# Kernel tuning notes

Measured on AMD Instinct MI355X. Metric: run time of the kernel, lower is better.

Reference implementation:

```python
import jax, jax.numpy as jnp
import numpy as np

D_MODEL = 1024
HEAD_DIM = 128
SEQ_LEN = 4096
BATCH = 4


def setup_inputs() -> dict:
    key = jax.random.key(0)
    kx, kq, kk, kv, ko = jax.random.split(key, 5)
    s = 1.0 / np.sqrt(D_MODEL)
    so = 1.0 / np.sqrt(HEAD_DIM)
    return {
        "x": jax.random.normal(kx, (SEQ_LEN, BATCH, D_MODEL), dtype=jnp.float32),
        "Wq": jax.random.uniform(kq, (HEAD_DIM, D_MODEL), jnp.float32, -s, s),
        "Wk": jax.random.uniform(kk, (HEAD_DIM, D_MODEL), jnp.float32, -s, s),
        "Wv": jax.random.uniform(kv, (HEAD_DIM, D_MODEL), jnp.float32, -s, s),
        "Wo": jax.random.uniform(ko, (D_MODEL, HEAD_DIM), jnp.float32, -so, so),
    }


def reference(x, Wq, Wk, Wv, Wo):
    # x: (S, B, D)
    S = x.shape[0]
    scale = Wq.shape[0] ** (-0.5)  # head_dim ** -0.5
    # Projections (Linear: x @ W.T) -> (B, S, H)
    Q = jnp.einsum('sbd,hd->bsh', x, Wq)
    K = jnp.einsum('sbd,hd->bsh', x, Wk)
    V = jnp.einsum('sbd,hd->bsh', x, Wv)
    scores = jnp.einsum('bqh,bkh->bqk', Q, K) * scale  # (B, S, S)
    causal = jnp.tril(jnp.ones((S, S), dtype=bool))
    scores = jnp.where(causal[None], scores, -jnp.inf)
    attn = jax.nn.softmax(scores, axis=-1)
    attn = jnp.nan_to_num(attn, nan=0.0)
    out = jnp.einsum('bqk,bkh->bqh', attn, V)  # (B, S, H)
    # out_proj then back to (S, B, D)
    return jnp.einsum('bsh,dh->sbd', out, Wo)
```

## Files before the change

### kernel.cpp

```cpp
#include <hip/hip_runtime.h>
#include <hip/hip_bf16.h>

#define S_LEN 4096
#define BATCH 4
#define DMODEL 1024
#define HDIM 128
#define NSLOT 4

typedef __attribute__((ext_vector_type(8))) short short8;
typedef __attribute__((ext_vector_type(4))) short short4v;
typedef __attribute__((ext_vector_type(4))) float float4v;
typedef __attribute__((ext_vector_type(16))) float float16v;
typedef __attribute__((ext_vector_type(4))) int int4v;

#define MASKVAL (-3.0e38f)
#define MINIT   (-1.0e30f)

static __device__ __forceinline__ unsigned short f2bf(float f) {
    __hip_bfloat16 h = __float2bfloat16(f);
    return *reinterpret_cast<unsigned short*>(&h);
}
static __device__ __forceinline__ unsigned short f2h(float f) {
    _Float16 h = (_Float16)f; return *reinterpret_cast<unsigned short*>(&h);
}
static __device__ __forceinline__ float h2f(unsigned short u) {
    _Float16 h = *reinterpret_cast<_Float16*>(&u); return (float)h;
}

__global__ __launch_bounds__(256) void xprep_kernel(
    const float* __restrict__ x, unsigned short* __restrict__ xf)
{
    int n = blockIdx.x * 256 + threadIdx.x;
    int b = n >> 17;
    int rem = n & 131071;
    int sb = rem >> 10;
    int rem2 = rem & 1023;
    int kq = rem2 >> 4;
    int grp = rem2 & 15;
    int lane0 = grp * 4;
    int par = grp >> 3;
    int s0 = lane0 & 31;
    int k = kq * 16 + par * 8;

    short8 hv[4];
#pragma unroll
    for (int r = 0; r < 4; r++) {
        int s = sb * 32 + s0 + r;
        const float* src = &x[((size_t)s * BATCH + b) * DMODEL + k];
        float4 v0 = *reinterpret_cast<const float4*>(src);
        float4 v1 = *reinterpret_cast<const float4*>(src + 4);
        short8 h;
        h[0] = (short)f2bf(v0.x); h[1] = (short)f2bf(v0.y);
        h[2] = (short)f2bf(v0.z); h[3] = (short)f2bf(v0.w);
        h[4] = (short)f2bf(v1.x); h[5] = (short)f2bf(v1.y);
        h[6] = (short)f2bf(v1.z); h[7] = (short)f2bf(v1.w);
        hv[r] = h;
    }
    size_t addr = (((size_t)b * 128 + sb) * 64 + kq) * 512 + (size_t)lane0 * 8;
#pragma unroll
    for (int r = 0; r < 4; r++)
        *reinterpret_cast<short8*>(xf + addr + r * 8) = hv[r];
}

__global__ __launch_bounds__(256) void wprep_kernel(
    const float* __restrict__ Wq, const float* __restrict__ Wk,
    const float* __restrict__ Wv, unsigned short* __restrict__ Wqf,
    unsigned short* __restrict__ Wkf, unsigned short* __restrict__ Wvf)
{
    const int which = blockIdx.y;
    const float* W = (which == 0) ? Wq : (which == 1) ? Wk : Wv;
    unsigned short* Wf = (which == 0) ? Wqf : (which == 1) ? Wkf : Wvf;
    int n = blockIdx.x * 256 + threadIdx.x;
    int d = n >> 7, k8 = n & 127;
    const float* src = &W[(size_t)d * DMODEL + k8 * 8];
    float4 v0 = *reinterpret_cast<const float4*>(src);
    float4 v1 = *reinterpret_cast<const float4*>(src + 4);
    short8 h;
    h[0] = (short)f2bf(v0.x); h[1] = (short)f2bf(v0.y);
    h[2] = (short)f2bf(v0.z); h[3] = (short)f2bf(v0.w);
    h[4] = (short)f2bf(v1.x); h[5] = (short)f2bf(v1.y);
    h[6] = (short)f2bf(v1.z); h[7] = (short)f2bf(v1.w);
    size_t addr = (((size_t)(d >> 5)) * 64 + (k8 >> 1)) * 512
                + (size_t)(((d & 31) + 32 * (k8 & 1)) * 8);
    *reinterpret_cast<short8*>(Wf + addr) = h;
}

__global__ __launch_bounds__(256, 4) void qkv_gemm_kernel(
    const unsigned short* __restrict__ xf, const unsigned short* __restrict__ Wqf,
    const unsigned short* __restrict__ Wkf, const unsigned short* __restrict__ Wvf,
    unsigned short* __restrict__ Qf, unsigned short* __restrict__ Kf,
    unsigned short* __restrict__ Vf)
{
    __shared__ float cacc[2 * 4096];

    const int t = threadIdx.x;
    const int w = t >> 6;
    const int lane = t & 63;
    const int hi = lane >> 5;
    const int tloc = w & 1;
    const int half = w >> 1;
    const int tile = blockIdx.x * 2 + tloc;
    const int which = tile >> 9;
    const int rem = tile & 511;
    const int b = rem >> 7;
    const int sblk = rem & 127;

    const unsigned short* Wf = (which == 0) ? Wqf : (which == 1) ? Wkf : Wvf;
    const unsigned short* xp =
        xf + (((size_t)b * 128 + sblk) * 64 + half * 32) * 512 + lane * 8;
    const unsigned short* wp = Wf + (size_t)half * 32 * 512 + lane * 8;

    float16v acc[4];
#pragma unroll
    for (int i = 0; i < 4; i++)
#pragma unroll
        for (int r = 0; r < 16; r++) acc[i][r] = 0.f;

    if (which != 2) {
#pragma unroll 2
        for (int ks = 0; ks < 32; ks++) {
            short8 xv = *reinterpret_cast<const short8*>(xp + ks * 512);
#pragma unroll
            for (int db = 0; db < 4; db++) {
                short8 wv = *reinterpret_cast<const short8*>(
                    wp + (size_t)(db * 64 + ks) * 512);
                acc[db] = __builtin_amdgcn_mfma_f32_32x32x16_bf16(
                    wv, xv, acc[db], 0, 0, 0);
            }
        }
    } else {
#pragma unroll 2
        for (int ks = 0; ks < 32; ks++) {
            short8 xv = *reinterpret_cast<const short8*>(xp + ks * 512);
#pragma unroll
            for (int hb = 0; hb < 4; hb++) {
                short8 wv = *reinterpret_cast<const short8*>(
                    wp + (size_t)(hb * 64 + ks) * 512);
                acc[hb] = __builtin_amdgcn_mfma_f32_32x32x16_bf16(
                    xv, wv, acc[hb], 0, 0, 0);
            }
        }
    }

    float* my = cacc + tloc * 4096;
    if (half == 1) {
#pragma unroll
        for (int db = 0; db < 4; db++)
#pragma unroll
            for (int rc = 0; rc < 4; rc++) {
                float4v v;
#pragma unroll
                for (int j = 0; j < 4; j++) v[j] = acc[db][rc * 4 + j];
                *reinterpret_cast<float4v*>(
                    my + (db * 4 + rc) * 256 + lane * 4) = v;
            }
    }
    __syncthreads();
    if (half != 0) return;

#pragma unroll
    for (int db = 0; db < 4; db++)
#pragma unroll
        for (int rc = 0; rc < 4; rc++) {
            float4v v = *reinterpret_cast<const float4v*>(
                my + (db * 4 + rc) * 256 + lane * 4);
#pragma unroll
            for (int j = 0; j < 4; j++) acc[db][rc * 4 + j] += v[j];
        }

    if (which != 2) {
        unsigned short* Of = (which == 0) ? Qf : Kf;
        const float scale = (which == 0) ? 0.08838834764831845f : 1.0f;
#pragma unroll
        for (int db = 0; db < 4; db++)
#pragma unroll
            for (int g = 0; g < 4; g++) {
                int f = db * 2 + (g >> 1);
                size_t addr = (((size_t)b * 128 + sblk) * 8 + f) * 512
                            + (size_t)(((lane & 31) + 32 * (g & 1)) * 8 + 4 * hi);
                short4v ov;
#pragma unroll
                for (int j = 0; j < 4; j++)
                    ov[j] = (short)f2bf(acc[db][g * 4 + j] * scale);
                *reinterpret_cast<short4v*>(Of + addr) = ov;
            }
    } else {
#pragma unroll
        for (int hb = 0; hb < 4; hb++)
#pragma unroll
            for (int g = 0; g < 4; g++) {
                int kt16 = sblk * 2 + (g >> 1);
                size_t addr = (((size_t)b * 256 + kt16) * 4 + hb) * 512
                            + (size_t)(((lane & 31) + 32 * (g & 1)) * 8 + 4 * hi);
                short4v ov;
#pragma unroll
                for (int j = 0; j < 4; j++)
                    ov[j] = (short)f2bf(acc[hb][g * 4 + j]);
                *reinterpret_cast<short4v*>(Vf + addr) = ov;
            }
    }
}

__global__ __launch_bounds__(256) void attn_kernel(
    const unsigned short* __restrict__ Qf, const unsigned short* __restrict__ Kf,
    const unsigned short* __restrict__ Vf, unsigned short* __restrict__ Opart,
    float* __restrict__ Mpart, float* __restrict__ Lpart)
{
    const int t = threadIdx.x;
    const int w = t >> 6;
    const int lane = t & 63;
    const int l31 = lane & 31;
    const int hi = lane >> 5;

    const int i = blockIdx.x;
    const int xx = i & 7, j = i >> 3;
    const int b = xx >> 1;
    const int p = j * 2 + (xx & 1);
    const int qt = 31 - (p & 31);
    const int c = p >> 5;

    const int nkv = 2 * (qt + 1);
    const int csize = (nkv + NSLOT - 1) / NSLOT;
    const int lo = c * csize;
    const int hic = min(lo + csize, nkv);
    if (lo >= hic) return;

    const int qb = qt * 128;
    const int qrow = qb + w * 32 + l31;

    const unsigned short* qp =
        Qf + (((size_t)b * 128 + (qt * 4 + w)) * 8) * 512 + lane * 8;
    short8 qf[8];
#pragma unroll
    for (int f = 0; f < 8; f++)
        qf[f] = *reinterpret_cast<const short8*>(qp + f * 512);

    const unsigned short* kbase =
        Kf + (size_t)b * (S_LEN / 32) * 8 * 512 + lane * 8;
    const unsigned short* vbase =
        Vf + (size_t)b * (S_LEN / 16) * 4 * 512 + lane * 8;

    float m_run = MINIT, l_run = 0.f;
    float16v o[4];
#pragma unroll
    for (int hb = 0; hb < 4; hb++)
#pragma unroll
        for (int r = 0; r < 16; r++) o[hb][r] = 0.f;

    for (int ti = lo; ti < hic; ti++) {
        const int kvb = ti * 64;
        const unsigned short* kp = kbase + (size_t)ti * 8192;

        float16v s0, s1;
#pragma unroll
        for (int r = 0; r < 16; r++) { s0[r] = 0.f; s1[r] = 0.f; }
#pragma unroll
        for (int f = 0; f < 8; f++) {
            short8 k0 = *reinterpret_cast<const short8*>(kp + f * 512);
            short8 k1 = *reinterpret_cast<const short8*>(kp + 4096 + f * 512);
            s0 = __builtin_amdgcn_mfma_f32_32x32x16_bf16(k0, qf[f], s0, 0, 0, 0);
            s1 = __builtin_amdgcn_mfma_f32_32x32x16_bf16(k1, qf[f], s1, 0, 0, 0);
        }

        if (kvb + 63 > qb + w * 32) {
#pragma unroll
            for (int r = 0; r < 16; r++) {
                int kv0 = kvb + (r & 3) + 8 * (r >> 2) + 4 * hi;
                if (kv0 > qrow) s0[r] = MASKVAL;
                if (kv0 + 32 > qrow) s1[r] = MASKVAL;
            }
        }

        float pmax = s0[0];
#pragma unroll
        for (int r = 1; r < 16; r++) pmax = fmaxf(pmax, s0[r]);
#pragma unroll
        for (int r = 0; r < 16; r++) pmax = fmaxf(pmax, s1[r]);
        pmax = fmaxf(pmax, __shfl_xor(pmax, 32));
        float mnew = fmaxf(m_run, pmax);
        float alpha = __expf(m_run - mnew);
        m_run = mnew;
#pragma unroll
        for (int r = 0; r < 16; r++) s0[r] = __expf(s0[r] - mnew);
#pragma unroll
        for (int r = 0; r < 16; r++) s1[r] = __expf(s1[r] - mnew);
        float sum = 0.f;
#pragma unroll
        for (int r = 0; r < 16; r++) sum += s0[r] + s1[r];
        sum += __shfl_xor(sum, 32);
        l_run = l_run * alpha + sum;
#pragma unroll
        for (int hb = 0; hb < 4; hb++) o[hb] = o[hb] * alpha;

        const unsigned short* vp = vbase + (size_t)ti * 8192;
#pragma unroll
        for (int tw = 0; tw < 4; tw++) {
            float pv[8];
#pragma unroll
            for (int jj = 0; jj < 8; jj++)
                pv[jj] = (tw < 2) ? ((tw & 1) ? s0[8 + jj] : s0[jj])
                                  : ((tw & 1) ? s1[8 + jj] : s1[jj]);
            unsigned int A  = (unsigned int)f2bf(pv[0]) | ((unsigned int)f2bf(pv[1]) << 16);
            unsigned int Bw = (unsigned int)f2bf(pv[2]) | ((unsigned int)f2bf(pv[3]) << 16);
            unsigned int C  = (unsigned int)f2bf(pv[4]) | ((unsigned int)f2bf(pv[5]) << 16);
            unsigned int D  = (unsigned int)f2bf(pv[6]) | ((unsigned int)f2bf(pv[7]) << 16);
            unsigned int y1 = (unsigned int)__shfl_xor((int)(hi ? A : C), 32);
            unsigned int y2 = (unsigned int)__shfl_xor((int)(hi ? Bw : D), 32);
            int4v pw;
            pw[0] = (int)(hi ? y1 : A);
            pw[1] = (int)(hi ? y2 : Bw);
            pw[2] = (int)(hi ? C : y1);
            pw[3] = (int)(hi ? D : y2);
            union { int4v iv; short8 s; } pu; pu.iv = pw;
#pragma unroll
            for (int hb = 0; hb < 4; hb++) {
                short8 vf = *reinterpret_cast<const short8*>(
                    vp + (tw * 4 + hb) * 512);
                o[hb] = __builtin_amdgcn_mfma_f32_32x32x16_bf16(vf, pu.s, o[hb], 0, 0, 0);
            }
        }
    }

    const size_t R0 = (size_t)(c * BATCH + b) * S_LEN;
    const float inv = (l_run > 0.f) ? 1.f / l_run : 0.f;
#pragma unroll
    for (int hb = 0; hb < 4; hb++)
#pragma unroll
        for (int g = 0; g < 4; g++) {
            int h0 = hb * 32 + g * 8 + hi * 4;
            short4v ov;
#pragma unroll
            for (int jj = 0; jj < 4; jj++)
                ov[jj] = (short)f2h(o[hb][g * 4 + jj] * inv);
            *reinterpret_cast<short4v*>(&Opart[(R0 + qrow) * HDIM + h0]) = ov;
        }
    if (hi == 0) { Mpart[R0 + qrow] = m_run; Lpart[R0 + qrow] = l_run; }
}

__global__ __launch_bounds__(256) void combine_kernel(
    const unsigned short* __restrict__ Opart, const float* __restrict__ Mpart,
    const float* __restrict__ Lpart, unsigned short* __restrict__ Ob)
{
    const int BS = BATCH * S_LEN;
    int idx = blockIdx.x * 256 + threadIdx.x;
    int r = idx >> 4, hc = (idx & 15) * 8;
    int q = r & (S_LEN - 1);
    int qt = q >> 7;
    int nkv = 2 * (qt + 1);
    int csize = (nkv + NSLOT - 1) / NSLOT;
    int cnt = (nkv + csize - 1) / csize;

    float m = -INFINITY;
    for (int j = 0; j < cnt; j++) m = fmaxf(m, Mpart[j * BS + r]);
    float wsum = 0.f;
    float acc[8];
#pragma unroll
    for (int e = 0; e < 8; e++) acc[e] = 0.f;
    for (int j = 0; j < cnt; j++) {
        float wj = __expf(Mpart[j * BS + r] - m) * Lpart[j * BS + r];
        wsum += wj;
        short8 o = *reinterpret_cast<const short8*>(
            &Opart[((size_t)j * BS + r) * HDIM + hc]);
#pragma unroll
        for (int e = 0; e < 8; e++) acc[e] += wj * h2f((unsigned short)o[e]);
    }
    float inv = 1.f / wsum;
    short8 ob;
#pragma unroll
    for (int e = 0; e < 8; e++) ob[e] = (short)f2bf(acc[e] * inv);
    *reinterpret_cast<short8*>(&Ob[(size_t)r * HDIM + hc]) = ob;
}

__global__ __launch_bounds__(256) void out_proj_kernel(
    const unsigned short* __restrict__ Ob, const float* __restrict__ Wo,
    float* __restrict__ out)
{
    __shared__ unsigned short As[128 * 128];
    __shared__ unsigned short Bs[128 * 128];

    const int t = threadIdx.x;
    const int lane = t & 63, w = t >> 6;
    const int l15 = lane & 15, l4 = lane >> 4;
    const int wr = (w >> 1) * 64, wc = (w & 1) * 64;
    const int s0 = blockIdx.x * 128;
    const int d0 = blockIdx.y * 128;
    const int b = blockIdx.z;

#pragma unroll
    for (int p = 0; p < 8; p++) {
        int e = p * 2048 + t * 8;
        int r = e >> 7, h = e & 127;
        short8 v = *reinterpret_cast<const short8*>(
            &Ob[((size_t)b * S_LEN + s0 + r) * HDIM + h]);
        int off = (r * 256 + h * 2) ^ ((r & 7) << 4);
        *reinterpret_cast<short8*>(reinterpret_cast<char*>(As) + off) = v;
    }
#pragma unroll
    for (int p = 0; p < 16; p++) {
        int e = p * 1024 + t * 4;
        int r = e >> 7, h = e & 127;
        float4 v = *reinterpret_cast<const float4*>(&Wo[(size_t)(d0 + r) * HDIM + h]);
        short4v hh;
        hh[0] = (short)f2bf(v.x); hh[1] = (short)f2bf(v.y);
        hh[2] = (short)f2bf(v.z); hh[3] = (short)f2bf(v.w);
        int off = (r * 256 + h * 2) ^ ((r & 7) << 4);
        *reinterpret_cast<short4v*>(reinterpret_cast<char*>(Bs) + off) = hh;
    }
    __syncthreads();

    float4v acc[4][4];
#pragma unroll
    for (int i = 0; i < 4; i++)
#pragma unroll
        for (int j = 0; j < 4; j++) acc[i][j] = (float4v){0.f, 0.f, 0.f, 0.f};

#pragma unroll
    for (int kk = 0; kk < 4; kk++) {
        short8 a[4], bf[4];
#pragma unroll
        for (int mi = 0; mi < 4; mi++) {
            int row = wr + mi * 16 + l15;
            int off = (row * 256 + (kk * 32 + l4 * 8) * 2) ^ ((row & 7) << 4);
            a[mi] = *reinterpret_cast<const short8*>(
                reinterpret_cast<const char*>(As) + off);
        }
#pragma unroll
        for (int ni = 0; ni < 4; ni++) {
            int row = wc + ni * 16 + l15;
            int off = (row * 256 + (kk * 32 + l4 * 8) * 2) ^ ((row & 7) << 4);
            bf[ni] = *reinterpret_cast<const short8*>(
                reinterpret_cast<const char*>(Bs) + off);
        }
#pragma unroll
        for (int mi = 0; mi < 4; mi++)
#pragma unroll
            for (int ni = 0; ni < 4; ni++)
                acc[mi][ni] = __builtin_amdgcn_mfma_f32_16x16x32_bf16(
                    a[mi], bf[ni], acc[mi][ni], 0, 0, 0);
    }

#pragma unroll
    for (int mi = 0; mi < 4; mi++)
#pragma unroll
        for (int ni = 0; ni < 4; ni++)
#pragma unroll
            for (int r = 0; r < 4; r++) {
                int s = s0 + wr + mi * 16 + l4 * 4 + r;
                int d = d0 + wc + ni * 16 + l15;
                out[((size_t)s * BATCH + b) * DMODEL + d] = acc[mi][ni][r];
            }
}

extern "C" void kernel_launch(void* const* d_in, const int* in_sizes, int n_in,
                              void* d_out, int out_size, void* d_ws, size_t ws_size,
                              hipStream_t stream) {
    const float* x  = (const float*)d_in[0];
    const float* Wq = (const float*)d_in[1];
    const float* Wk = (const float*)d_in[2];
    const float* Wv = (const float*)d_in[3];
    const float* Wo = (const float*)d_in[4];
    float* out = (float*)d_out;

    const size_t BS = (size_t)BATCH * S_LEN;
    unsigned short* xf    = (unsigned short*)d_ws;
    unsigned short* Opart = (unsigned short*)d_ws;
    float* Mpart = (float*)((char*)d_ws + (16u << 20));
    float* Lpart = Mpart + NSLOT * BS;
    unsigned short* Wqf = (unsigned short*)((char*)d_ws + (32u << 20));
    unsigned short* Wkf = Wqf + 131072;
    unsigned short* Wvf = Wkf + 131072;
    unsigned short* Qf  = Wvf + 131072;
    unsigned short* Kf  = Qf + 2097152;
    unsigned short* Vf  = Kf + 2097152;
    unsigned short* Ob  = Vf + 2097152;

    xprep_kernel<<<2048, 256, 0, stream>>>(x, xf);
    wprep_kernel<<<dim3(64, 3), 256, 0, stream>>>(Wq, Wk, Wv, Wqf, Wkf, Wvf);
    qkv_gemm_kernel<<<768, 256, 0, stream>>>(xf, Wqf, Wkf, Wvf, Qf, Kf, Vf);
    attn_kernel<<<512, 256, 0, stream>>>(Qf, Kf, Vf, Opart, Mpart, Lpart);
    combine_kernel<<<1024, 256, 0, stream>>>(Opart, Mpart, Lpart, Ob);
    out_proj_kernel<<<dim3(32, 8, BATCH), 256, 0, stream>>>(Ob, Wo, out);
}
```

Before: 147.0 us.

## Pipeline K/V loads, split attention into fixed 8-block chunks, lazy rescale

Measured after the change: 126.7 us. 1.16x faster.

```diff
diff --git a/kernel.cpp b/kernel.cpp
--- a/kernel.cpp
+++ b/kernel.cpp
@@ -5,7 +5,7 @@
 #define BATCH 4
 #define DMODEL 1024
 #define HDIM 128
-#define NSLOT 4
+#define NSLOT 8
 
 typedef __attribute__((ext_vector_type(8))) short short8;
 typedef __attribute__((ext_vector_type(4))) short short4v;
@@ -25,6 +25,24 @@
 }
 static __device__ __forceinline__ float h2f(unsigned short u) {
     _Float16 h = *reinterpret_cast<_Float16*>(&u); return (float)h;
+}
+static __device__ __forceinline__ short8 ldf(const unsigned short* p) {
+    return *reinterpret_cast<const short8*>(p);
+}
+static __device__ __forceinline__ short8 pack_p(const float* pv, int hi) {
+    unsigned int A  = (unsigned int)f2bf(pv[0]) | ((unsigned int)f2bf(pv[1]) << 16);
+    unsigned int Bw = (unsigned int)f2bf(pv[2]) | ((unsigned int)f2bf(pv[3]) << 16);
+    unsigned int C  = (unsigned int)f2bf(pv[4]) | ((unsigned int)f2bf(pv[5]) << 16);
+    unsigned int D  = (unsigned int)f2bf(pv[6]) | ((unsigned int)f2bf(pv[7]) << 16);
+    unsigned int y1 = (unsigned int)__shfl_xor((int)(hi ? A : C), 32);
+    unsigned int y2 = (unsigned int)__shfl_xor((int)(hi ? Bw : D), 32);
+    int4v pw;
+    pw[0] = (int)(hi ? y1 : A);
+    pw[1] = (int)(hi ? y2 : Bw);
+    pw[2] = (int)(hi ? C : y1);
+    pw[3] = (int)(hi ? D : y2);
+    union { int4v iv; short8 s; } pu; pu.iv = pw;
+    return pu.s;
 }
 
 __global__ __launch_bounds__(256) void xprep_kernel(
@@ -85,7 +103,7 @@
     *reinterpret_cast<short8*>(Wf + addr) = h;
 }
 
-__global__ __launch_bounds__(256, 4) void qkv_gemm_kernel(
+__global__ __launch_bounds__(256) void qkv_gemm_kernel(
     const unsigned short* __restrict__ xf, const unsigned short* __restrict__ Wqf,
     const unsigned short* __restrict__ Wkf, const unsigned short* __restrict__ Wvf,
     unsigned short* __restrict__ Qf, unsigned short* __restrict__ Kf,
@@ -116,29 +134,38 @@
 #pragma unroll
         for (int r = 0; r < 16; r++) acc[i][r] = 0.f;
 
-    if (which != 2) {
-#pragma unroll 2
+    {
+        short8 xA = ldf(xp);
+        short8 wA[4];
+#pragma unroll
+        for (int d4 = 0; d4 < 4; d4++) wA[d4] = ldf(wp + (size_t)(d4 * 64) * 512);
         for (int ks = 0; ks < 32; ks++) {
-            short8 xv = *reinterpret_cast<const short8*>(xp + ks * 512);
-#pragma unroll
-            for (int db = 0; db < 4; db++) {
-                short8 wv = *reinterpret_cast<const short8*>(
-                    wp + (size_t)(db * 64 + ks) * 512);
-                acc[db] = __builtin_amdgcn_mfma_f32_32x32x16_bf16(
-                    wv, xv, acc[db], 0, 0, 0);
-            }
-        }
-    } else {
-#pragma unroll 2
-        for (int ks = 0; ks < 32; ks++) {
-            short8 xv = *reinterpret_cast<const short8*>(xp + ks * 512);
-#pragma unroll
-            for (int hb = 0; hb < 4; hb++) {
-                short8 wv = *reinterpret_cast<const short8*>(
-                    wp + (size_t)(hb * 64 + ks) * 512);
-                acc[hb] = __builtin_amdgcn_mfma_f32_32x32x16_bf16(
-                    xv, wv, acc[hb], 0, 0, 0);
-            }
+            short8 xB = xA;
+            short8 wB[4];
+#pragma unroll
+            for (int d4 = 0; d4 < 4; d4++) wB[d4] = wA[d4];
+            if (ks < 31) {
+                xB = ldf(xp + (ks + 1) * 512);
+#pragma unroll
+                for (int d4 = 0; d4 < 4; d4++)
+                    wB[d4] = ldf(wp + (size_t)(d4 * 64 + ks + 1) * 512);
+            }
+            __builtin_amdgcn_s_setprio(1);
+            if (which != 2) {
+#pragma unroll
+                for (int d4 = 0; d4 < 4; d4++)
+                    acc[d4] = __builtin_amdgcn_mfma_f32_32x32x16_bf16(
+                        wA[d4], xA, acc[d4], 0, 0, 0);
+            } else {
+#pragma unroll
+                for (int d4 = 0; d4 < 4; d4++)
+                    acc[d4] = __builtin_amdgcn_mfma_f32_32x32x16_bf16(
+                        xA, wA[d4], acc[d4], 0, 0, 0);
+            }
+            __builtin_amdgcn_s_setprio(0);
+            xA = xB;
+#pragma unroll
+            for (int d4 = 0; d4 < 4; d4++) wA[d4] = wB[d4];
         }
     }
 
@@ -213,27 +240,27 @@
     const int hi = lane >> 5;
 
     const int i = blockIdx.x;
-    const int xx = i & 7, j = i >> 3;
+    const int xx = i & 7;
     const int b = xx >> 1;
-    const int p = j * 2 + (xx & 1);
+    const int p = (i >> 3) * 2 + (xx & 1);
     const int qt = 31 - (p & 31);
     const int c = p >> 5;
 
     const int nkv = 2 * (qt + 1);
-    const int csize = (nkv + NSLOT - 1) / NSLOT;
-    const int lo = c * csize;
-    const int hic = min(lo + csize, nkv);
-    if (lo >= hic) return;
+    const int lo = c * 8;
+    if (lo >= nkv) return;
+    const int hic = min(lo + 8, nkv);
 
     const int qb = qt * 128;
     const int qrow = qb + w * 32 + l31;
+    const int lastblk = (qb + w * 32 + 31) >> 6;
+    const int myhi = min(hic, lastblk + 1);
 
     const unsigned short* qp =
         Qf + (((size_t)b * 128 + (qt * 4 + w)) * 8) * 512 + lane * 8;
     short8 qf[8];
 #pragma unroll
-    for (int f = 0; f < 8; f++)
-        qf[f] = *reinterpret_cast<const short8*>(qp + f * 512);
+    for (int f = 0; f < 8; f++) qf[f] = ldf(qp + f * 512);
 
     const unsigned short* kbase =
         Kf + (size_t)b * (S_LEN / 32) * 8 * 512 + lane * 8;
@@ -247,20 +274,49 @@
 #pragma unroll
         for (int r = 0; r < 16; r++) o[hb][r] = 0.f;
 
-    for (int ti = lo; ti < hic; ti++) {
+    for (int ti = lo; ti < myhi; ti++) {
         const int kvb = ti * 64;
         const unsigned short* kp = kbase + (size_t)ti * 8192;
+        const unsigned short* vp = vbase + (size_t)ti * 8192;
+
+        short8 ka[4], kb[4], va[4], vb[4];
+#pragma unroll
+        for (int j = 0; j < 4; j++) ka[j] = ldf(kp + j * 512);
+#pragma unroll
+        for (int j = 0; j < 4; j++) kb[j] = ldf(kp + (4 + j) * 512);
 
         float16v s0, s1;
 #pragma unroll
         for (int r = 0; r < 16; r++) { s0[r] = 0.f; s1[r] = 0.f; }
-#pragma unroll
-        for (int f = 0; f < 8; f++) {
-            short8 k0 = *reinterpret_cast<const short8*>(kp + f * 512);
-            short8 k1 = *reinterpret_cast<const short8*>(kp + 4096 + f * 512);
-            s0 = __builtin_amdgcn_mfma_f32_32x32x16_bf16(k0, qf[f], s0, 0, 0, 0);
-            s1 = __builtin_amdgcn_mfma_f32_32x32x16_bf16(k1, qf[f], s1, 0, 0, 0);
-        }
+
+        __builtin_amdgcn_s_setprio(1);
+#pragma unroll
+        for (int j = 0; j < 4; j++)
+            s0 = __builtin_amdgcn_mfma_f32_32x32x16_bf16(ka[j], qf[j], s0, 0, 0, 0);
+        __builtin_amdgcn_s_setprio(0);
+#pragma unroll
+        for (int j = 0; j < 4; j++) ka[j] = ldf(kp + 4096 + j * 512);
+        __builtin_amdgcn_s_setprio(1);
+#pragma unroll
+        for (int j = 0; j < 4; j++)
+            s0 = __builtin_amdgcn_mfma_f32_32x32x16_bf16(kb[j], qf[4 + j], s0, 0, 0, 0);
+        __builtin_amdgcn_s_setprio(0);
+#pragma unroll
+        for (int j = 0; j < 4; j++) kb[j] = ldf(kp + 4096 + (4 + j) * 512);
+        __builtin_amdgcn_s_setprio(1);
+#pragma unroll
+        for (int j = 0; j < 4; j++)
+            s1 = __builtin_amdgcn_mfma_f32_32x32x16_bf16(ka[j], qf[j], s1, 0, 0, 0);
+        __builtin_amdgcn_s_setprio(0);
+#pragma unroll
+        for (int j = 0; j < 4; j++) va[j] = ldf(vp + j * 512);
+        __builtin_amdgcn_s_setprio(1);
+#pragma unroll
+        for (int j = 0; j < 4; j++)
+            s1 = __builtin_amdgcn_mfma_f32_32x32x16_bf16(kb[j], qf[4 + j], s1, 0, 0, 0);
+        __builtin_amdgcn_s_setprio(0);
+#pragma unroll
+        for (int j = 0; j < 4; j++) vb[j] = ldf(vp + (4 + j) * 512);
 
         if (kvb + 63 > qb + w * 32) {
 #pragma unroll
@@ -271,54 +327,65 @@
             }
         }
 
-        float pmax = s0[0];
-#pragma unroll
-        for (int r = 1; r < 16; r++) pmax = fmaxf(pmax, s0[r]);
-#pragma unroll
-        for (int r = 0; r < 16; r++) pmax = fmaxf(pmax, s1[r]);
-        pmax = fmaxf(pmax, __shfl_xor(pmax, 32));
-        float mnew = fmaxf(m_run, pmax);
-        float alpha = __expf(m_run - mnew);
-        m_run = mnew;
-#pragma unroll
-        for (int r = 0; r < 16; r++) s0[r] = __expf(s0[r] - mnew);
-#pragma unroll
-        for (int r = 0; r < 16; r++) s1[r] = __expf(s1[r] - mnew);
-        float sum = 0.f;
-#pragma unroll
-        for (int r = 0; r < 16; r++) sum += s0[r] + s1[r];
-        sum += __shfl_xor(sum, 32);
-        l_run = l_run * alpha + sum;
-#pragma unroll
-        for (int hb = 0; hb < 4; hb++) o[hb] = o[hb] * alpha;
-
-        const unsigned short* vp = vbase + (size_t)ti * 8192;
-#pragma unroll
-        for (int tw = 0; tw < 4; tw++) {
-            float pv[8];
-#pragma unroll
-            for (int jj = 0; jj < 8; jj++)
-                pv[jj] = (tw < 2) ? ((tw & 1) ? s0[8 + jj] : s0[jj])
-                                  : ((tw & 1) ? s1[8 + jj] : s1[jj]);
-            unsigned int A  = (unsigned int)f2bf(pv[0]) | ((unsigned int)f2bf(pv[1]) << 16);
-            unsigned int Bw = (unsigned int)f2bf(pv[2]) | ((unsigned int)f2bf(pv[3]) << 16);
-            unsigned int C  = (unsigned int)f2bf(pv[4]) | ((unsigned int)f2bf(pv[5]) << 16);
-            unsigned int D  = (unsigned int)f2bf(pv[6]) | ((unsigned int)f2bf(pv[7]) << 16);
-            unsigned int y1 = (unsigned int)__shfl_xor((int)(hi ? A : C), 32);
-            unsigned int y2 = (unsigned int)__shfl_xor((int)(hi ? Bw : D), 32);
-            int4v pw;
-            pw[0] = (int)(hi ? y1 : A);
-            pw[1] = (int)(hi ? y2 : Bw);
-            pw[2] = (int)(hi ? C : y1);
-            pw[3] = (int)(hi ? D : y2);
-            union { int4v iv; short8 s; } pu; pu.iv = pw;
-#pragma unroll
-            for (int hb = 0; hb < 4; hb++) {
-                short8 vf = *reinterpret_cast<const short8*>(
-                    vp + (tw * 4 + hb) * 512);
-                o[hb] = __builtin_amdgcn_mfma_f32_32x32x16_bf16(vf, pu.s, o[hb], 0, 0, 0);
-            }
-        }
+        float mx[16];
+#pragma unroll
+        for (int r = 0; r < 16; r++) mx[r] = fmaxf(s0[r], s1[r]);
+#pragma unroll
+        for (int st = 8; st >= 1; st >>= 1)
+#pragma unroll
+            for (int r = 0; r < st; r++) mx[r] = fmaxf(mx[r], mx[r + st]);
+        float pmax = fmaxf(mx[0], __shfl_xor(mx[0], 32));
+        if (!__all(pmax - m_run <= 8.0f)) {
+            float mnew = fmaxf(m_run, pmax);
+            float alpha = __expf(m_run - mnew);
+            l_run *= alpha;
+#pragma unroll
+            for (int hb = 0; hb < 4; hb++) o[hb] = o[hb] * alpha;
+            m_run = mnew;
+        }
+#pragma unroll
+        for (int r = 0; r < 16; r++) s0[r] = __expf(s0[r] - m_run);
+#pragma unroll
+        for (int r = 0; r < 16; r++) s1[r] = __expf(s1[r] - m_run);
+        float sm[16];
+#pragma unroll
+        for (int r = 0; r < 16; r++) sm[r] = s0[r] + s1[r];
+#pragma unroll
+        for (int st = 8; st >= 1; st >>= 1)
+#pragma unroll
+            for (int r = 0; r < st; r++) sm[r] += sm[r + st];
+        l_run += sm[0] + __shfl_xor(sm[0], 32);
+
+        float t0[8], t1[8], t2[8], t3[8];
+#pragma unroll
+        for (int j = 0; j < 8; j++) { t0[j] = s0[j]; t1[j] = s0[8 + j]; }
+#pragma unroll
+        for (int j = 0; j < 8; j++) { t2[j] = s1[j]; t3[j] = s1[8 + j]; }
+
+#pragma unroll
+        for (int j = 0; j < 4; j++) ka[j] = ldf(vp + (8 + j) * 512);
+        short8 p0 = pack_p(t0, hi);
+        __builtin_amdgcn_s_setprio(1);
+#pragma unroll
+        for (int hb = 0; hb < 4; hb++)
+            o[hb] = __builtin_amdgcn_mfma_f32_32x32x16_bf16(va[hb], p0, o[hb], 0, 0, 0);
+        __builtin_amdgcn_s_setprio(0);
+#pragma unroll
+        for (int j = 0; j < 4; j++) kb[j] = ldf(vp + (12 + j) * 512);
+        short8 p1 = pack_p(t1, hi);
+        __builtin_amdgcn_s_setprio(1);
+#pragma unroll
+        for (int hb = 0; hb < 4; hb++)
+            o[hb] = __builtin_amdgcn_mfma_f32_32x32x16_bf16(vb[hb], p1, o[hb], 0, 0, 0);
+        short8 p2 = pack_p(t2, hi);
+#pragma unroll
+        for (int hb = 0; hb < 4; hb++)
+            o[hb] = __builtin_amdgcn_mfma_f32_32x32x16_bf16(ka[hb], p2, o[hb], 0, 0, 0);
+        short8 p3 = pack_p(t3, hi);
+#pragma unroll
+        for (int hb = 0; hb < 4; hb++)
+            o[hb] = __builtin_amdgcn_mfma_f32_32x32x16_bf16(kb[hb], p3, o[hb], 0, 0, 0);
+        __builtin_amdgcn_s_setprio(0);
     }
 
     const size_t R0 = (size_t)(c * BATCH + b) * S_LEN;
@@ -347,8 +414,7 @@
     int q = r & (S_LEN - 1);
     int qt = q >> 7;
     int nkv = 2 * (qt + 1);
-    int csize = (nkv + NSLOT - 1) / NSLOT;
-    int cnt = (nkv + csize - 1) / csize;
+    int cnt = (nkv + 7) >> 3;
 
     float m = -INFINITY;
     for (int j = 0; j < cnt; j++) m = fmaxf(m, Mpart[j * BS + r]);
@@ -464,9 +530,9 @@
     const size_t BS = (size_t)BATCH * S_LEN;
     unsigned short* xf    = (unsigned short*)d_ws;
     unsigned short* Opart = (unsigned short*)d_ws;
-    float* Mpart = (float*)((char*)d_ws + (16u << 20));
+    float* Mpart = (float*)((char*)d_ws + (32u << 20));
     float* Lpart = Mpart + NSLOT * BS;
-    unsigned short* Wqf = (unsigned short*)((char*)d_ws + (32u << 20));
+    unsigned short* Wqf = (unsigned short*)((char*)d_ws + (33u << 20));
     unsigned short* Wkf = Wqf + 131072;
     unsigned short* Wvf = Wkf + 131072;
     unsigned short* Qf  = Wvf + 131072;
@@ -477,7 +543,7 @@
     xprep_kernel<<<2048, 256, 0, stream>>>(x, xf);
     wprep_kernel<<<dim3(64, 3), 256, 0, stream>>>(Wq, Wk, Wv, Wqf, Wkf, Wvf);
     qkv_gemm_kernel<<<768, 256, 0, stream>>>(xf, Wqf, Wkf, Wvf, Qf, Kf, Vf);
-    attn_kernel<<<512, 256, 0, stream>>>(Qf, Kf, Vf, Opart, Mpart, Lpart);
+    attn_kernel<<<1024, 256, 0, stream>>>(Qf, Kf, Vf, Opart, Mpart, Lpart);
     combine_kernel<<<1024, 256, 0, stream>>>(Opart, Mpart, Lpart, Ob);
     out_proj_kernel<<<dim3(32, 8, BATCH), 256, 0, stream>>>(Ob, Wo, out);
 }
```
